# Kernel optimization log

Measured on AMD Instinct MI355X. Metric: run time of the kernel, lower is better.

Reference implementation:

```python
import jax, jax.numpy as jnp
import numpy as np

HEADS = 12
D_MODEL = 768
D_TOKEN = D_MODEL // HEADS


def setup_inputs() -> dict:
    key = jax.random.key(0)
    ks = jax.random.split(key, 11)
    B, S, D = 2, 4096, D_MODEL
    scale = 1.0 / np.sqrt(D)
    return {
        "q": jax.random.normal(ks[0], (B, S, D), jnp.float32),
        "k": jax.random.normal(ks[1], (B, S, D), jnp.float32),
        "v": jax.random.normal(ks[2], (B, S, D), jnp.float32),
        "Wq": jax.random.normal(ks[3], (D, D), jnp.float32) * scale,
        "bq": jnp.zeros((D,), jnp.float32),
        "Wk": jax.random.normal(ks[4], (D, D), jnp.float32) * scale,
        "bk": jnp.zeros((D,), jnp.float32),
        "Wv": jax.random.normal(ks[5], (D, D), jnp.float32) * scale,
        "bv": jnp.zeros((D,), jnp.float32),
        "Wo": jax.random.normal(ks[6], (D, D), jnp.float32) * scale,
        "bo": jnp.zeros((D,), jnp.float32),
    }


def reference(q, k, v, Wq, bq, Wk, bk, Wv, bv, Wo, bo):
    B, S, D = q.shape
    H, Dh = HEADS, D_TOKEN
    # Linear projections (torch Linear: x @ W.T + b), split into heads: [B,H,S,Dh]
    qh = (q @ Wq.T + bq).reshape(B, S, H, Dh).transpose(0, 2, 1, 3)
    kh = (k @ Wk.T + bk).reshape(B, S, H, Dh).transpose(0, 2, 1, 3)
    vh = (v @ Wv.T + bv).reshape(B, S, H, Dh).transpose(0, 2, 1, 3)
    # Scaled dot-product attention (full O(S^2) scores, as the original does)
    scores = jnp.einsum("bhqd,bhkd->bhqk", qh, kh) / jnp.sqrt(
        jnp.asarray(Dh, qh.dtype))
    attn = jax.nn.softmax(scores, axis=-1)
    ctx = jnp.einsum("bhqk,bhkd->bhqd", attn, vh)
    ctx = ctx.transpose(0, 2, 1, 3).reshape(B, S, D)
    return ctx @ Wo.T + bo
```

## Files before the change

### kernel.cpp

```cpp
#include <hip/hip_runtime.h>


typedef __attribute__((ext_vector_type(4))) float f32x4;
typedef __attribute__((ext_vector_type(16))) float f32x16;
typedef __attribute__((ext_vector_type(8))) __bf16 bf16x8;
typedef __attribute__((ext_vector_type(2))) int i32x2;
typedef __attribute__((ext_vector_type(4))) unsigned u32x4;
using u16 = unsigned short;
using u32 = unsigned;

__device__ __forceinline__ u16 f2bf(float x) {
  __bf16 h = (__bf16)x;
  return __builtin_bit_cast(u16, h);
}
__device__ __forceinline__ u32 pk2(float lo, float hi) {
  u32 r;
  asm("v_cvt_pk_bf16_f32 %0, %1, %2" : "=v"(r) : "v"(lo), "v"(hi));
  return r;
}
__device__ __forceinline__ void gload16(u16* ldsDst, const u16* gSrc) {
  __builtin_amdgcn_global_load_lds(
      (const __attribute__((address_space(1))) void*)gSrc,
      (__attribute__((address_space(3))) void*)ldsDst, 16, 0, 0);
}
__device__ __forceinline__ f32x4 mfma16(bf16x8 a, bf16x8 b, f32x4 c) {
  return __builtin_amdgcn_mfma_f32_16x16x32_bf16(a, b, c, 0, 0, 0);
}
__device__ __forceinline__ f32x16 mfma32(bf16x8 a, bf16x8 b, f32x16 c) {
  return __builtin_amdgcn_mfma_f32_32x32x16_bf16(a, b, c, 0, 0, 0);
}
__device__ __forceinline__ bf16x8 ld8(const u16* p) { return *(const bf16x8*)p; }

__global__ void cvt_hi(const float4* __restrict__ in0, u16* o0,
                       const float4* __restrict__ in1, u16* o1,
                       const float4* __restrict__ in2, u16* o2,
                       const float4* __restrict__ in3, u16* o3, int n4) {
  const float4* in = in0; u16* o = o0;
  if (blockIdx.y == 1) { in = in1; o = o1; }
  else if (blockIdx.y == 2) { in = in2; o = o2; }
  else if (blockIdx.y == 3) { in = in3; o = o3; }
  const int stride = gridDim.x * blockDim.x;
  for (int i = blockIdx.x * blockDim.x + threadIdx.x; i < n4; i += stride) {
    float4 x = in[i];
    *(ushort4*)&o[i * 4] = make_ushort4(f2bf(x.x), f2bf(x.y), f2bf(x.z), f2bf(x.w));
  }
}

__global__ __launch_bounds__(256, 2) void gemm_qkv(
    const float* __restrict__ Aq, const float* __restrict__ Ak,
    const float* __restrict__ Av,
    const u16* __restrict__ wq, const u16* __restrict__ wk, const u16* __restrict__ wv,
    const float* __restrict__ bq, const float* __restrict__ bk,
    const float* __restrict__ bv,
    u16* __restrict__ oq, u16* __restrict__ ok, u16* __restrict__ ov,
    float qscale) {
  constexpr int K = 768;
  constexpr int BUF = 12288;
  __shared__ __align__(16) u16 lds[2 * BUF];
  const int z = blockIdx.z;
  const float* A = (z == 0) ? Aq : (z == 1) ? Ak : Av;
  const u16* Bh = (z == 0) ? wq : (z == 1) ? wk : wv;
  const float* bias = (z == 0) ? bq : (z == 1) ? bk : bv;
  u16* C = (z == 0) ? oq : (z == 1) ? ok : ov;
  const float scale = (z == 0) ? qscale : 1.f;
  const bool vmode = (z == 2);

  const int tid = threadIdx.x, lane = tid & 63, w = tid >> 6;
  const int wr = w >> 1, wc = w & 1;
  const int g = lane >> 4, la = lane & 15;
  const int m0 = blockIdx.x * 128, n0 = blockIdx.y * 128;

  f32x4 acc[4][4] = {};

  auto stage = [&](int buf, int kt) {
    const int k0 = kt * 32;
    u16* base = &lds[buf * BUF];
#pragma unroll
    for (int j = 0; j < 4; ++j) {
      const int i = w * 4 + j;
      const int r = i * 8 + (lane >> 3);
      const int c = (lane & 7) ^ ((lane >> 3) & 7);
      gload16(base + i * 512, (const u16*)(A + (size_t)(m0 + r) * K + k0 + c * 4));
    }
#pragma unroll
    for (int j = 0; j < 2; ++j) {
      const int t = w * 2 + j;
      const int s = t * 64 + lane;
      const int sr = s >> 3, ph = s & 7, ch = ph ^ (sr & 7);
      const int row = sr * 2 + (ch >> 2), c = ch & 3;
      gload16(base + 8192 + t * 512, Bh + (size_t)(n0 + row) * K + k0 + c * 8);
    }
  };
  auto rdfragA = [&](const float* baseF, int row, int gg) -> bf16x8 {
    const int x = row & 7;
    const f32x4 u = *(const f32x4*)(baseF + row * 32 + (((2 * gg) ^ x) << 2));
    const f32x4 v = *(const f32x4*)(baseF + row * 32 + (((2 * gg + 1) ^ x) << 2));
    u32x4 wq_ = {pk2(u[0], u[1]), pk2(u[2], u[3]), pk2(v[0], v[1]), pk2(v[2], v[3])};
    return __builtin_bit_cast(bf16x8, wq_);
  };
  auto rdfragB = [&](const u16* base, int row, int c) -> bf16x8 {
    const int sr = row >> 1;
    const int ph = (((row & 1) << 2) | c) ^ (sr & 7);
    return ld8(base + sr * 64 + ph * 8);
  };

  stage(0, 0);
  __syncthreads();
  constexpr int nk = K / 32;
  int cur = 0;
  for (int kt = 0; kt < nk; ++kt) {
    if (kt + 1 < nk) stage(cur ^ 1, kt + 1);
    const float* aF = (const float*)&lds[cur * BUF];
    const u16* bB = &lds[cur * BUF + 8192];
    bf16x8 aH[4], bH[4];
#pragma unroll
    for (int ni = 0; ni < 4; ++ni) bH[ni] = rdfragB(bB, wc * 64 + ni * 16 + la, g);
#pragma unroll
    for (int mi = 0; mi < 4; ++mi) aH[mi] = rdfragA(aF, wr * 64 + mi * 16 + la, g);
#pragma unroll
    for (int mi = 0; mi < 4; ++mi)
#pragma unroll
      for (int ni = 0; ni < 4; ++ni)
        acc[mi][ni] = mfma16(aH[mi], bH[ni], acc[mi][ni]);
    __syncthreads();
    cur ^= 1;
  }

#pragma unroll
  for (int mi = 0; mi < 4; ++mi) {
    const int mbase = m0 + wr * 64 + mi * 16 + g * 4;
#pragma unroll
    for (int ni = 0; ni < 4; ++ni) {
      const int n = n0 + wc * 64 + ni * 16 + la;
      const float bv_ = bias[n];
#pragma unroll
      for (int r = 0; r < 4; ++r) {
        const int m = mbase + r;
        const float y = (acc[mi][ni][r] + bv_) * scale;
        const int bb = m >> 12, s = m & 4095, hh = n >> 6, dh = n & 63;
        if (!vmode)
          C[((size_t)(bb * 12 + hh) * 4096 + s) * 64 + dh] = f2bf(y);
        else
          C[((size_t)(bb * 12 + hh) * 64 + dh) * 4096 + s] = f2bf(y);
      }
    }
  }
}

__global__ __launch_bounds__(256, 2) void gemm_out(
    const u16* __restrict__ A, const u16* __restrict__ Bh,
    const float* __restrict__ bias, float* __restrict__ Cf) {
  constexpr int K = 768, N = 768;
  constexpr int BUF = 8192;
  __shared__ __align__(16) u16 lds[2 * BUF];
  const int tid = threadIdx.x, lane = tid & 63, w = tid >> 6;
  const int wr = w >> 1, wc = w & 1;
  const int g = lane >> 4, la = lane & 15;
  const int m0 = blockIdx.x * 128, n0 = blockIdx.y * 128;

  f32x4 acc[4][4] = {};

  auto stage = [&](int buf, int kt) {
    const int k0 = kt * 32;
#pragma unroll
    for (int j = 0; j < 2; ++j) {
      const int t = w * 2 + j;
      const int s = t * 64 + lane;
      const int sr = s >> 3, ph = s & 7, ch = ph ^ (sr & 7);
      const int row = sr * 2 + (ch >> 2), c = ch & 3;
      const int gofs = k0 + c * 8;
      u16* base = &lds[buf * BUF];
      gload16(base + t * 512, A + (size_t)(m0 + row) * K + gofs);
      gload16(base + 4096 + t * 512, Bh + (size_t)(n0 + row) * K + gofs);
    }
  };
  auto rdfrag = [&](const u16* base, int row, int c) -> bf16x8 {
    const int sr = row >> 1;
    const int ph = (((row & 1) << 2) | c) ^ (sr & 7);
    return ld8(base + sr * 64 + ph * 8);
  };

  stage(0, 0);
  __syncthreads();
  constexpr int nk = K / 32;
  int cur = 0;
  for (int kt = 0; kt < nk; ++kt) {
    if (kt + 1 < nk) stage(cur ^ 1, kt + 1);
    const u16* bA = &lds[cur * BUF];
    bf16x8 aH[4], bH[4];
#pragma unroll
    for (int mi = 0; mi < 4; ++mi) aH[mi] = rdfrag(bA, wr * 64 + mi * 16 + la, g);
#pragma unroll
    for (int ni = 0; ni < 4; ++ni) bH[ni] = rdfrag(bA + 4096, wc * 64 + ni * 16 + la, g);
#pragma unroll
    for (int mi = 0; mi < 4; ++mi)
#pragma unroll
      for (int ni = 0; ni < 4; ++ni)
        acc[mi][ni] = mfma16(aH[mi], bH[ni], acc[mi][ni]);
    __syncthreads();
    cur ^= 1;
  }

#pragma unroll
  for (int mi = 0; mi < 4; ++mi) {
    const int mbase = m0 + wr * 64 + mi * 16 + g * 4;
#pragma unroll
    for (int ni = 0; ni < 4; ++ni) {
      const int n = n0 + wc * 64 + ni * 16 + la;
      const float bv_ = bias[n];
#pragma unroll
      for (int r = 0; r < 4; ++r)
        Cf[(size_t)(mbase + r) * N + n] = acc[mi][ni][r] + bv_;
    }
  }
}

__global__ __launch_bounds__(256, 3) void flash_attn(
    const u16* __restrict__ Q, const u16* __restrict__ Kt,
    const u16* __restrict__ Vt, u16* __restrict__ ctx) {
  __shared__ __align__(16) u16 lds[2 * 8192];
  const int tid = threadIdx.x, lane = tid & 63, w = tid >> 6;
  const int l5 = lane & 31, hi = lane >> 5;
  const int bh = blockIdx.y, b = bh / 12, h = bh % 12;
  const int q0 = blockIdx.x * 128 + w * 32;
  const size_t kbase = (size_t)bh * 4096 * 64;
  const size_t vbase = (size_t)bh * 64 * 4096;

  bf16x8 aQ[4];
#pragma unroll
  for (int ks = 0; ks < 4; ++ks)
    aQ[ks] = ld8(Q + kbase + (size_t)(q0 + l5) * 64 + ks * 16 + hi * 8);

  f32x16 accO0 = {}, accO1 = {}, accLP = {};
  f32x16 M4;
#pragma unroll
  for (int i = 0; i < 16; ++i) M4[i] = -4.0f;
  const u32x4 onebits = {0x3F803F80u, 0x3F803F80u, 0x3F803F80u, 0x3F803F80u};
  const bf16x8 ones = __builtin_bit_cast(bf16x8, onebits);

  int aK0[4], aK1[4];
  {
    const int r0 = l5, f0 = (r0 & 7) ^ (r0 >> 3);
    const int r1 = 32 + l5, f1 = (r1 & 7) ^ (r1 >> 3);
#pragma unroll
    for (int ks = 0; ks < 4; ++ks) {
      aK0[ks] = r0 * 64 + (((ks * 2 + hi) ^ f0) << 3);
      aK1[ks] = r1 * 64 + (((ks * 2 + hi) ^ f1) << 3);
    }
  }

  const u16 *gk0, *gk1, *gv0, *gv1;
  int dK0, dK1, dV0, dV1;
  {
    const int t0 = w * 2, s0_ = t0 * 64 + lane;
    const int sr0 = s0_ >> 3, c0 = (s0_ & 7) ^ ((sr0 & 7) ^ (sr0 >> 3));
    gk0 = Kt + kbase + (size_t)sr0 * 64 + c0 * 8;
    gv0 = Vt + vbase + (size_t)sr0 * 4096 + c0 * 8;
    dK0 = t0 * 512; dV0 = 4096 + t0 * 512;
    const int t1 = t0 + 1, s1_ = t1 * 64 + lane;
    const int sr1 = s1_ >> 3, c1 = (s1_ & 7) ^ ((sr1 & 7) ^ (sr1 >> 3));
    gk1 = Kt + kbase + (size_t)sr1 * 64 + c1 * 8;
    gv1 = Vt + vbase + (size_t)sr1 * 4096 + c1 * 8;
    dK1 = t1 * 512; dV1 = 4096 + t1 * 512;
  }

  auto stage = [&](int bufbase, int tile) {
    gload16(&lds[bufbase + dK0], gk0 + (size_t)tile * 4096);
    gload16(&lds[bufbase + dK1], gk1 + (size_t)tile * 4096);
    gload16(&lds[bufbase + dV0], gv0 + tile * 64);
    gload16(&lds[bufbase + dV1], gv1 + tile * 64);
  };

  auto body = [&](const int B0) {
    f32x16 s0, s1;
    {
      bf16x8 k0 = ld8(&lds[B0 + aK0[0]]);
      bf16x8 k1 = ld8(&lds[B0 + aK1[0]]);
      s0 = mfma32(k0, aQ[0], M4);
      s1 = mfma32(k1, aQ[0], M4);
    }
#pragma unroll
    for (int ks = 1; ks < 4; ++ks) {
      bf16x8 k0 = ld8(&lds[B0 + aK0[ks]]);
      bf16x8 k1 = ld8(&lds[B0 + aK1[ks]]);
      s0 = mfma32(k0, aQ[ks], s0);
      s1 = mfma32(k1, aQ[ks], s1);
    }
#pragma unroll
    for (int ct = 0; ct < 2; ++ct) {
      const f32x16 sv = ct ? s1 : s0;
      float p[16];
#pragma unroll
      for (int i = 0; i < 16; ++i) p[i] = __builtin_exp2f(sv[i]);
      u32 W[4][2];
#pragma unroll
      for (int qd = 0; qd < 4; ++qd) {
        W[qd][0] = pk2(p[qd * 4 + 0], p[qd * 4 + 1]);
        W[qd][1] = pk2(p[qd * 4 + 2], p[qd * 4 + 3]);
      }
#pragma unroll
      for (int s2 = 0; s2 < 2; ++s2) {
        i32x2 r1 = __builtin_amdgcn_permlane32_swap((int)W[2 * s2][0], (int)W[2 * s2 + 1][0], false, false);
        i32x2 r2 = __builtin_amdgcn_permlane32_swap((int)W[2 * s2][1], (int)W[2 * s2 + 1][1], false, false);
        u32x4 wq = {(u32)r1.x, (u32)r2.x, (u32)r1.y, (u32)r2.y};
        const bf16x8 pb = __builtin_bit_cast(bf16x8, wq);
        const int ksv = ct * 2 + s2;
        bf16x8 v0 = ld8(&lds[B0 + 4096 + aK0[ksv]]);
        bf16x8 v1 = ld8(&lds[B0 + 4096 + aK1[ksv]]);
        accO0 = mfma32(v0, pb, accO0);
        accO1 = mfma32(v1, pb, accO1);
        accLP = mfma32(ones, pb, accLP);
      }
    }
  };

  stage(0, 0);
  __syncthreads();
#pragma unroll 1
  for (int t2 = 0; t2 < 32; ++t2) {
    stage(8192, 2 * t2 + 1);
    body(0);
    __syncthreads();
    if (t2 < 31) stage(0, 2 * t2 + 2);
    body(8192);
    __syncthreads();
  }

  const float inv = __builtin_amdgcn_rcpf(accLP[0]);
  u16* crow = ctx + ((size_t)b * 4096 + q0 + l5) * 768 + h * 64;
#pragma unroll
  for (int dt = 0; dt < 2; ++dt) {
    const f32x16 a = dt ? accO1 : accO0;
#pragma unroll
    for (int rq = 0; rq < 4; ++rq) {
      const int d0 = dt * 32 + 8 * rq + 4 * hi;
      uint2 st;
      st.x = pk2(a[rq * 4 + 0] * inv, a[rq * 4 + 1] * inv);
      st.y = pk2(a[rq * 4 + 2] * inv, a[rq * 4 + 3] * inv);
      *(uint2*)&crow[d0] = st;
    }
  }
}

extern "C" void kernel_launch(void* const* d_in, const int* in_sizes, int n_in,
                              void* d_out, int out_size, void* d_ws, size_t ws_size,
                              hipStream_t stream) {
  constexpr int NQKV = 2 * 4096 * 768;
  constexpr int NW = 768 * 768;
  const float* q = (const float*)d_in[0];
  const float* k = (const float*)d_in[1];
  const float* v = (const float*)d_in[2];
  const float* Wq = (const float*)d_in[3];
  const float* bq = (const float*)d_in[4];
  const float* Wk = (const float*)d_in[5];
  const float* bk = (const float*)d_in[6];
  const float* Wv = (const float*)d_in[7];
  const float* bv = (const float*)d_in[8];
  const float* Wo = (const float*)d_in[9];
  const float* bo = (const float*)d_in[10];

  char* p = (char*)d_ws;
  auto take = [&](size_t n) -> u16* {
    u16* r = (u16*)p;
    p += (n * 2 + 255) & ~(size_t)255;
    return r;
  };
  u16 *wq_h = take(NW), *wk_h = take(NW), *wv_h = take(NW), *wo_h = take(NW);
  u16 *qh = take(NQKV), *kh = take(NQKV), *vt = take(NQKV), *ctx = take(NQKV);

  cvt_hi<<<dim3(288, 4), 256, 0, stream>>>(
      (const float4*)Wq, wq_h, (const float4*)Wk, wk_h,
      (const float4*)Wv, wv_h, (const float4*)Wo, wo_h, NW / 4);

  const float qscale = 0.18033688011112042f;
  gemm_qkv<<<dim3(64, 6, 3), 256, 0, stream>>>(
      q, k, v, wq_h, wk_h, wv_h, bq, bk, bv, qh, kh, vt, qscale);
  flash_attn<<<dim3(32, 24), 256, 0, stream>>>(qh, kh, vt, ctx);
  gemm_out<<<dim3(64, 6), 256, 0, stream>>>(ctx, wo_h, bo, (float*)d_out);
}
```

Baseline: 230.8 us.

## Split attention over key halves, merge partials, and convert weights in-GEMM

The weight-conversion kernel is removed. The QKV and output GEMMs now stage fp32 weights straight into LDS and convert them to bf16 during fragment reads. Flash attention is split across two key halves (grid z=2) with smaller 32-key tiles and higher occupancy. Each half writes unnormalized fp32 partial outputs and row sums, and a new merge kernel adds them, normalizes, and writes bf16 context. This adds fp32 partial traffic, one extra launch, and doubled LDS for weights in exchange for more parallel attention blocks and one less launch.

```diff
diff --git a/kernel.cpp b/kernel.cpp
--- a/kernel.cpp
+++ b/kernel.cpp
@@ -31,35 +31,21 @@
 }
 __device__ __forceinline__ bf16x8 ld8(const u16* p) { return *(const bf16x8*)p; }
 
-__global__ void cvt_hi(const float4* __restrict__ in0, u16* o0,
-                       const float4* __restrict__ in1, u16* o1,
-                       const float4* __restrict__ in2, u16* o2,
-                       const float4* __restrict__ in3, u16* o3, int n4) {
-  const float4* in = in0; u16* o = o0;
-  if (blockIdx.y == 1) { in = in1; o = o1; }
-  else if (blockIdx.y == 2) { in = in2; o = o2; }
-  else if (blockIdx.y == 3) { in = in3; o = o3; }
-  const int stride = gridDim.x * blockDim.x;
-  for (int i = blockIdx.x * blockDim.x + threadIdx.x; i < n4; i += stride) {
-    float4 x = in[i];
-    *(ushort4*)&o[i * 4] = make_ushort4(f2bf(x.x), f2bf(x.y), f2bf(x.z), f2bf(x.w));
-  }
-}
-
 __global__ __launch_bounds__(256, 2) void gemm_qkv(
     const float* __restrict__ Aq, const float* __restrict__ Ak,
     const float* __restrict__ Av,
-    const u16* __restrict__ wq, const u16* __restrict__ wk, const u16* __restrict__ wv,
+    const float* __restrict__ Wq, const float* __restrict__ Wk,
+    const float* __restrict__ Wv,
     const float* __restrict__ bq, const float* __restrict__ bk,
     const float* __restrict__ bv,
     u16* __restrict__ oq, u16* __restrict__ ok, u16* __restrict__ ov,
     float qscale) {
   constexpr int K = 768;
-  constexpr int BUF = 12288;
+  constexpr int BUF = 16384;
   __shared__ __align__(16) u16 lds[2 * BUF];
   const int z = blockIdx.z;
   const float* A = (z == 0) ? Aq : (z == 1) ? Ak : Av;
-  const u16* Bh = (z == 0) ? wq : (z == 1) ? wk : wv;
+  const float* Bf = (z == 0) ? Wq : (z == 1) ? Wk : Wv;
   const float* bias = (z == 0) ? bq : (z == 1) ? bk : bv;
   u16* C = (z == 0) ? oq : (z == 1) ? ok : ov;
   const float scale = (z == 0) ? qscale : 1.f;
@@ -75,33 +61,22 @@
   auto stage = [&](int buf, int kt) {
     const int k0 = kt * 32;
     u16* base = &lds[buf * BUF];
+    const int r8 = lane >> 3;
+    const int c = (lane & 7) ^ r8;
 #pragma unroll
     for (int j = 0; j < 4; ++j) {
       const int i = w * 4 + j;
-      const int r = i * 8 + (lane >> 3);
-      const int c = (lane & 7) ^ ((lane >> 3) & 7);
+      const int r = i * 8 + r8;
       gload16(base + i * 512, (const u16*)(A + (size_t)(m0 + r) * K + k0 + c * 4));
-    }
-#pragma unroll
-    for (int j = 0; j < 2; ++j) {
-      const int t = w * 2 + j;
-      const int s = t * 64 + lane;
-      const int sr = s >> 3, ph = s & 7, ch = ph ^ (sr & 7);
-      const int row = sr * 2 + (ch >> 2), c = ch & 3;
-      gload16(base + 8192 + t * 512, Bh + (size_t)(n0 + row) * K + k0 + c * 8);
-    }
-  };
-  auto rdfragA = [&](const float* baseF, int row, int gg) -> bf16x8 {
+      gload16(base + 8192 + i * 512, (const u16*)(Bf + (size_t)(n0 + r) * K + k0 + c * 4));
+    }
+  };
+  auto rdfragF = [&](const float* baseF, int row, int gg) -> bf16x8 {
     const int x = row & 7;
     const f32x4 u = *(const f32x4*)(baseF + row * 32 + (((2 * gg) ^ x) << 2));
     const f32x4 v = *(const f32x4*)(baseF + row * 32 + (((2 * gg + 1) ^ x) << 2));
     u32x4 wq_ = {pk2(u[0], u[1]), pk2(u[2], u[3]), pk2(v[0], v[1]), pk2(v[2], v[3])};
     return __builtin_bit_cast(bf16x8, wq_);
-  };
-  auto rdfragB = [&](const u16* base, int row, int c) -> bf16x8 {
-    const int sr = row >> 1;
-    const int ph = (((row & 1) << 2) | c) ^ (sr & 7);
-    return ld8(base + sr * 64 + ph * 8);
   };
 
   stage(0, 0);
@@ -111,12 +86,12 @@
   for (int kt = 0; kt < nk; ++kt) {
     if (kt + 1 < nk) stage(cur ^ 1, kt + 1);
     const float* aF = (const float*)&lds[cur * BUF];
-    const u16* bB = &lds[cur * BUF + 8192];
+    const float* bF = (const float*)&lds[cur * BUF + 8192];
     bf16x8 aH[4], bH[4];
 #pragma unroll
-    for (int ni = 0; ni < 4; ++ni) bH[ni] = rdfragB(bB, wc * 64 + ni * 16 + la, g);
-#pragma unroll
-    for (int mi = 0; mi < 4; ++mi) aH[mi] = rdfragA(aF, wr * 64 + mi * 16 + la, g);
+    for (int ni = 0; ni < 4; ++ni) bH[ni] = rdfragF(bF, wc * 64 + ni * 16 + la, g);
+#pragma unroll
+    for (int mi = 0; mi < 4; ++mi) aH[mi] = rdfragF(aF, wr * 64 + mi * 16 + la, g);
 #pragma unroll
     for (int mi = 0; mi < 4; ++mi)
 #pragma unroll
@@ -148,10 +123,10 @@
 }
 
 __global__ __launch_bounds__(256, 2) void gemm_out(
-    const u16* __restrict__ A, const u16* __restrict__ Bh,
+    const u16* __restrict__ A, const float* __restrict__ Bf,
     const float* __restrict__ bias, float* __restrict__ Cf) {
   constexpr int K = 768, N = 768;
-  constexpr int BUF = 8192;
+  constexpr int BUF = 12288;
   __shared__ __align__(16) u16 lds[2 * BUF];
   const int tid = threadIdx.x, lane = tid & 63, w = tid >> 6;
   const int wr = w >> 1, wc = w & 1;
@@ -162,22 +137,35 @@
 
   auto stage = [&](int buf, int kt) {
     const int k0 = kt * 32;
+    u16* base = &lds[buf * BUF];
 #pragma unroll
     for (int j = 0; j < 2; ++j) {
       const int t = w * 2 + j;
       const int s = t * 64 + lane;
       const int sr = s >> 3, ph = s & 7, ch = ph ^ (sr & 7);
       const int row = sr * 2 + (ch >> 2), c = ch & 3;
-      const int gofs = k0 + c * 8;
-      u16* base = &lds[buf * BUF];
-      gload16(base + t * 512, A + (size_t)(m0 + row) * K + gofs);
-      gload16(base + 4096 + t * 512, Bh + (size_t)(n0 + row) * K + gofs);
-    }
-  };
-  auto rdfrag = [&](const u16* base, int row, int c) -> bf16x8 {
+      gload16(base + t * 512, A + (size_t)(m0 + row) * K + k0 + c * 8);
+    }
+    const int r8 = lane >> 3;
+    const int c = (lane & 7) ^ r8;
+#pragma unroll
+    for (int j = 0; j < 4; ++j) {
+      const int i = w * 4 + j;
+      const int r = i * 8 + r8;
+      gload16(base + 4096 + i * 512, (const u16*)(Bf + (size_t)(n0 + r) * K + k0 + c * 4));
+    }
+  };
+  auto rdfragA = [&](const u16* base, int row, int c) -> bf16x8 {
     const int sr = row >> 1;
     const int ph = (((row & 1) << 2) | c) ^ (sr & 7);
     return ld8(base + sr * 64 + ph * 8);
+  };
+  auto rdfragF = [&](const float* baseF, int row, int gg) -> bf16x8 {
+    const int x = row & 7;
+    const f32x4 u = *(const f32x4*)(baseF + row * 32 + (((2 * gg) ^ x) << 2));
+    const f32x4 v = *(const f32x4*)(baseF + row * 32 + (((2 * gg + 1) ^ x) << 2));
+    u32x4 wq_ = {pk2(u[0], u[1]), pk2(u[2], u[3]), pk2(v[0], v[1]), pk2(v[2], v[3])};
+    return __builtin_bit_cast(bf16x8, wq_);
   };
 
   stage(0, 0);
@@ -187,11 +175,12 @@
   for (int kt = 0; kt < nk; ++kt) {
     if (kt + 1 < nk) stage(cur ^ 1, kt + 1);
     const u16* bA = &lds[cur * BUF];
+    const float* bF = (const float*)&lds[cur * BUF + 4096];
     bf16x8 aH[4], bH[4];
 #pragma unroll
-    for (int mi = 0; mi < 4; ++mi) aH[mi] = rdfrag(bA, wr * 64 + mi * 16 + la, g);
-#pragma unroll
-    for (int ni = 0; ni < 4; ++ni) bH[ni] = rdfrag(bA + 4096, wc * 64 + ni * 16 + la, g);
+    for (int mi = 0; mi < 4; ++mi) aH[mi] = rdfragA(bA, wr * 64 + mi * 16 + la, g);
+#pragma unroll
+    for (int ni = 0; ni < 4; ++ni) bH[ni] = rdfragF(bF, wc * 64 + ni * 16 + la, g);
 #pragma unroll
     for (int mi = 0; mi < 4; ++mi)
 #pragma unroll
@@ -215,16 +204,18 @@
   }
 }
 
-__global__ __launch_bounds__(256, 3) void flash_attn(
+__global__ __launch_bounds__(256, 6) void flash_attn(
     const u16* __restrict__ Q, const u16* __restrict__ Kt,
-    const u16* __restrict__ Vt, u16* __restrict__ ctx) {
-  __shared__ __align__(16) u16 lds[2 * 8192];
+    const u16* __restrict__ Vt, float* __restrict__ opart,
+    float* __restrict__ lppart) {
+  __shared__ __align__(16) u16 lds[2 * 4096];
   const int tid = threadIdx.x, lane = tid & 63, w = tid >> 6;
   const int l5 = lane & 31, hi = lane >> 5;
-  const int bh = blockIdx.y, b = bh / 12, h = bh % 12;
+  const int bh = blockIdx.y, z = blockIdx.z;
   const int q0 = blockIdx.x * 128 + w * 32;
   const size_t kbase = (size_t)bh * 4096 * 64;
   const size_t vbase = (size_t)bh * 64 * 4096;
+  const int ko = z * 2048;
 
   bf16x8 aQ[4];
 #pragma unroll
@@ -238,79 +229,60 @@
   const u32x4 onebits = {0x3F803F80u, 0x3F803F80u, 0x3F803F80u, 0x3F803F80u};
   const bf16x8 ones = __builtin_bit_cast(bf16x8, onebits);
 
-  int aK0[4], aK1[4];
+  const int f0 = (l5 & 7) ^ (l5 >> 3);
+  int aK0[4], aV0[2], aV1[2];
+#pragma unroll
+  for (int ks = 0; ks < 4; ++ks)
+    aK0[ks] = l5 * 64 + (((ks * 2 + hi) ^ f0) << 3);
+#pragma unroll
+  for (int s2 = 0; s2 < 2; ++s2) {
+    aV0[s2] = 2048 + l5 * 64 + (((s2 * 2 + hi) ^ f0) << 3);
+    aV1[s2] = 2048 + l5 * 64 + (((4 + s2 * 2 + hi) ^ f0) << 3);
+  }
+
+  const u16 *gk, *gv;
+  int dK, dV;
   {
-    const int r0 = l5, f0 = (r0 & 7) ^ (r0 >> 3);
-    const int r1 = 32 + l5, f1 = (r1 & 7) ^ (r1 >> 3);
-#pragma unroll
-    for (int ks = 0; ks < 4; ++ks) {
-      aK0[ks] = r0 * 64 + (((ks * 2 + hi) ^ f0) << 3);
-      aK1[ks] = r1 * 64 + (((ks * 2 + hi) ^ f1) << 3);
-    }
-  }
-
-  const u16 *gk0, *gk1, *gv0, *gv1;
-  int dK0, dK1, dV0, dV1;
-  {
-    const int t0 = w * 2, s0_ = t0 * 64 + lane;
-    const int sr0 = s0_ >> 3, c0 = (s0_ & 7) ^ ((sr0 & 7) ^ (sr0 >> 3));
-    gk0 = Kt + kbase + (size_t)sr0 * 64 + c0 * 8;
-    gv0 = Vt + vbase + (size_t)sr0 * 4096 + c0 * 8;
-    dK0 = t0 * 512; dV0 = 4096 + t0 * 512;
-    const int t1 = t0 + 1, s1_ = t1 * 64 + lane;
-    const int sr1 = s1_ >> 3, c1 = (s1_ & 7) ^ ((sr1 & 7) ^ (sr1 >> 3));
-    gk1 = Kt + kbase + (size_t)sr1 * 64 + c1 * 8;
-    gv1 = Vt + vbase + (size_t)sr1 * 4096 + c1 * 8;
-    dK1 = t1 * 512; dV1 = 4096 + t1 * 512;
-  }
-
-  auto stage = [&](int bufbase, int tile) {
-    gload16(&lds[bufbase + dK0], gk0 + (size_t)tile * 4096);
-    gload16(&lds[bufbase + dK1], gk1 + (size_t)tile * 4096);
-    gload16(&lds[bufbase + dV0], gv0 + tile * 64);
-    gload16(&lds[bufbase + dV1], gv1 + tile * 64);
+    const int r = w * 8 + (lane >> 3);
+    const int fr = (r & 7) ^ (r >> 3);
+    const int cK = (lane & 7) ^ fr;
+    gk = Kt + kbase + (size_t)(ko + r) * 64 + cK * 8;
+    dK = w * 512;
+    const int cp = (lane & 7) ^ fr;
+    const int dd = r + 32 * (cp >> 2), cc = cp & 3;
+    gv = Vt + vbase + (size_t)dd * 4096 + ko + cc * 8;
+    dV = 2048 + w * 512;
+  }
+  auto stage = [&](int B0, int tile) {
+    gload16(&lds[B0 + dK], gk + (size_t)tile * 2048);
+    gload16(&lds[B0 + dV], gv + tile * 32);
   };
 
   auto body = [&](const int B0) {
-    f32x16 s0, s1;
-    {
-      bf16x8 k0 = ld8(&lds[B0 + aK0[0]]);
-      bf16x8 k1 = ld8(&lds[B0 + aK1[0]]);
-      s0 = mfma32(k0, aQ[0], M4);
-      s1 = mfma32(k1, aQ[0], M4);
-    }
-#pragma unroll
-    for (int ks = 1; ks < 4; ++ks) {
-      bf16x8 k0 = ld8(&lds[B0 + aK0[ks]]);
-      bf16x8 k1 = ld8(&lds[B0 + aK1[ks]]);
-      s0 = mfma32(k0, aQ[ks], s0);
-      s1 = mfma32(k1, aQ[ks], s1);
-    }
-#pragma unroll
-    for (int ct = 0; ct < 2; ++ct) {
-      const f32x16 sv = ct ? s1 : s0;
-      float p[16];
-#pragma unroll
-      for (int i = 0; i < 16; ++i) p[i] = __builtin_exp2f(sv[i]);
-      u32 W[4][2];
-#pragma unroll
-      for (int qd = 0; qd < 4; ++qd) {
-        W[qd][0] = pk2(p[qd * 4 + 0], p[qd * 4 + 1]);
-        W[qd][1] = pk2(p[qd * 4 + 2], p[qd * 4 + 3]);
-      }
-#pragma unroll
-      for (int s2 = 0; s2 < 2; ++s2) {
-        i32x2 r1 = __builtin_amdgcn_permlane32_swap((int)W[2 * s2][0], (int)W[2 * s2 + 1][0], false, false);
-        i32x2 r2 = __builtin_amdgcn_permlane32_swap((int)W[2 * s2][1], (int)W[2 * s2 + 1][1], false, false);
-        u32x4 wq = {(u32)r1.x, (u32)r2.x, (u32)r1.y, (u32)r2.y};
-        const bf16x8 pb = __builtin_bit_cast(bf16x8, wq);
-        const int ksv = ct * 2 + s2;
-        bf16x8 v0 = ld8(&lds[B0 + 4096 + aK0[ksv]]);
-        bf16x8 v1 = ld8(&lds[B0 + 4096 + aK1[ksv]]);
-        accO0 = mfma32(v0, pb, accO0);
-        accO1 = mfma32(v1, pb, accO1);
-        accLP = mfma32(ones, pb, accLP);
-      }
+    f32x16 s0 = mfma32(ld8(&lds[B0 + aK0[0]]), aQ[0], M4);
+#pragma unroll
+    for (int ks = 1; ks < 4; ++ks)
+      s0 = mfma32(ld8(&lds[B0 + aK0[ks]]), aQ[ks], s0);
+    float p[16];
+#pragma unroll
+    for (int i = 0; i < 16; ++i) p[i] = __builtin_exp2f(s0[i]);
+    u32 W[4][2];
+#pragma unroll
+    for (int qd = 0; qd < 4; ++qd) {
+      W[qd][0] = pk2(p[qd * 4 + 0], p[qd * 4 + 1]);
+      W[qd][1] = pk2(p[qd * 4 + 2], p[qd * 4 + 3]);
+    }
+#pragma unroll
+    for (int s2 = 0; s2 < 2; ++s2) {
+      i32x2 r1 = __builtin_amdgcn_permlane32_swap((int)W[2 * s2][0], (int)W[2 * s2 + 1][0], false, false);
+      i32x2 r2 = __builtin_amdgcn_permlane32_swap((int)W[2 * s2][1], (int)W[2 * s2 + 1][1], false, false);
+      u32x4 wq = {(u32)r1.x, (u32)r2.x, (u32)r1.y, (u32)r2.y};
+      const bf16x8 pb = __builtin_bit_cast(bf16x8, wq);
+      bf16x8 v0 = ld8(&lds[B0 + aV0[s2]]);
+      bf16x8 v1 = ld8(&lds[B0 + aV1[s2]]);
+      accO0 = mfma32(v0, pb, accO0);
+      accO1 = mfma32(v1, pb, accO1);
+      accLP = mfma32(ones, pb, accLP);
     }
   };
 
@@ -318,27 +290,53 @@
   __syncthreads();
 #pragma unroll 1
   for (int t2 = 0; t2 < 32; ++t2) {
-    stage(8192, 2 * t2 + 1);
+    stage(4096, 2 * t2 + 1);
     body(0);
     __syncthreads();
     if (t2 < 31) stage(0, 2 * t2 + 2);
-    body(8192);
+    body(4096);
     __syncthreads();
   }
 
-  const float inv = __builtin_amdgcn_rcpf(accLP[0]);
-  u16* crow = ctx + ((size_t)b * 4096 + q0 + l5) * 768 + h * 64;
+  const size_t obase = ((size_t)z * 768 + bh * 32 + blockIdx.x) * 8192;
 #pragma unroll
   for (int dt = 0; dt < 2; ++dt) {
     const f32x16 a = dt ? accO1 : accO0;
 #pragma unroll
-    for (int rq = 0; rq < 4; ++rq) {
-      const int d0 = dt * 32 + 8 * rq + 4 * hi;
-      uint2 st;
-      st.x = pk2(a[rq * 4 + 0] * inv, a[rq * 4 + 1] * inv);
-      st.y = pk2(a[rq * 4 + 2] * inv, a[rq * 4 + 3] * inv);
-      *(uint2*)&crow[d0] = st;
-    }
+    for (int rq = 0; rq < 4; ++rq)
+#pragma unroll
+      for (int j = 0; j < 4; ++j) {
+        const int d = dt * 32 + 8 * rq + 4 * hi + j;
+        opart[obase + (size_t)d * 128 + w * 32 + l5] = a[rq * 4 + j];
+      }
+  }
+  if (hi == 0)
+    lppart[(size_t)z * 98304 + (size_t)(bh * 32 + blockIdx.x) * 128 + w * 32 + l5] =
+        accLP[0];
+}
+
+__global__ void merge_halves(const float* __restrict__ opart,
+                             const float* __restrict__ lppart,
+                             u16* __restrict__ ctx) {
+  const int blk = blockIdx.x;
+  const int bh = blk >> 5, qt = blk & 31;
+  const int q = threadIdx.x;
+  const float l = lppart[(size_t)blk * 128 + q] + lppart[98304 + (size_t)blk * 128 + q];
+  const float inv = __builtin_amdgcn_rcpf(l);
+  const size_t o1 = (size_t)blk * 8192 + q;
+  const size_t o2 = o1 + 6291456;
+  const int b = bh / 12, h = bh % 12;
+  u16* crow = ctx + ((size_t)b * 4096 + qt * 128 + q) * 768 + h * 64;
+#pragma unroll
+  for (int d0 = 0; d0 < 8; ++d0) {
+    float o[8];
+#pragma unroll
+    for (int j = 0; j < 8; ++j) {
+      const size_t off = (size_t)(d0 * 8 + j) * 128;
+      o[j] = (opart[o1 + off] + opart[o2 + off]) * inv;
+    }
+    u32x4 pkv = {pk2(o[0], o[1]), pk2(o[2], o[3]), pk2(o[4], o[5]), pk2(o[6], o[7])};
+    *(u32x4*)&crow[d0 * 8] = pkv;
   }
 }
 
@@ -346,7 +344,6 @@
                               void* d_out, int out_size, void* d_ws, size_t ws_size,
                               hipStream_t stream) {
   constexpr int NQKV = 2 * 4096 * 768;
-  constexpr int NW = 768 * 768;
   const float* q = (const float*)d_in[0];
   const float* k = (const float*)d_in[1];
   const float* v = (const float*)d_in[2];
@@ -365,16 +362,14 @@
     p += (n * 2 + 255) & ~(size_t)255;
     return r;
   };
-  u16 *wq_h = take(NW), *wk_h = take(NW), *wv_h = take(NW), *wo_h = take(NW);
   u16 *qh = take(NQKV), *kh = take(NQKV), *vt = take(NQKV), *ctx = take(NQKV);
-
-  cvt_hi<<<dim3(288, 4), 256, 0, stream>>>(
-      (const float4*)Wq, wq_h, (const float4*)Wk, wk_h,
-      (const float4*)Wv, wv_h, (const float4*)Wo, wo_h, NW / 4);
+  float* opart = (float*)take(2u * 12582912u);
+  float* lppart = (float*)take(2u * 196608u);
 
   const float qscale = 0.18033688011112042f;
   gemm_qkv<<<dim3(64, 6, 3), 256, 0, stream>>>(
-      q, k, v, wq_h, wk_h, wv_h, bq, bk, bv, qh, kh, vt, qscale);
-  flash_attn<<<dim3(32, 24), 256, 0, stream>>>(qh, kh, vt, ctx);
-  gemm_out<<<dim3(64, 6), 256, 0, stream>>>(ctx, wo_h, bo, (float*)d_out);
-}
+      q, k, v, Wq, Wk, Wv, bq, bk, bv, qh, kh, vt, qscale);
+  flash_attn<<<dim3(32, 24, 2), 256, 0, stream>>>(qh, kh, vt, opart, lppart);
+  merge_halves<<<768, 128, 0, stream>>>(opart, lppart, ctx);
+  gemm_out<<<dim3(64, 6), 256, 0, stream>>>(ctx, Wo, bo, (float*)d_out);
+}
```

Result: slower. 481.2 us (+108.5%).
